# Performance work log

Measured on AMD Instinct MI355X. Metric: run time of the kernel, lower is better.

Reference implementation:

```python
import jax, jax.numpy as jnp
import numpy as np

B, C, H, W = 2, 512, 64, 64
G = 32          # GroupNorm groups
EPS = 1e-6


def setup_inputs() -> dict:
    key = jax.random.key(0)
    ks = jax.random.split(key, 10)
    s = 1.0 / np.sqrt(C)
    return {
        "x": jax.random.normal(ks[0], (B, C, H, W), dtype=jnp.float32),
        "gn_w": jnp.ones((C,), jnp.float32),
        "gn_b": jnp.zeros((C,), jnp.float32),
        "wq": jax.random.normal(ks[1], (C, C), jnp.float32) * s,
        "bq": jnp.zeros((C,), jnp.float32),
        "wk": jax.random.normal(ks[2], (C, C), jnp.float32) * s,
        "bk": jnp.zeros((C,), jnp.float32),
        "wv": jax.random.normal(ks[3], (C, C), jnp.float32) * s,
        "bv": jnp.zeros((C,), jnp.float32),
        "wo": jax.random.normal(ks[4], (C, C), jnp.float32) * s,
        "bo": jnp.zeros((C,), jnp.float32),
    }


def reference(x, gn_w, gn_b, wq, bq, wk, bk, wv, bv, wo, bo):
    b, c, h, w = x.shape
    n = h * w
    # GroupNorm(32, eps=1e-6, affine)
    xg = x.reshape(b, G, c // G, h, w)
    mu = xg.mean(axis=(2, 3, 4), keepdims=True)
    var = ((xg - mu) ** 2).mean(axis=(2, 3, 4), keepdims=True)
    hn = ((xg - mu) * jax.lax.rsqrt(var + EPS)).reshape(b, c, h, w)
    hn = hn * gn_w[None, :, None, None] + gn_b[None, :, None, None]
    # 1x1 convs == per-pixel linear over channels; tokens: b n c
    hf = hn.reshape(b, c, n)
    q = jnp.einsum('oc,bcn->bno', wq, hf) + bq  # [b, n, c]
    k = jnp.einsum('oc,bcn->bno', wk, hf) + bk
    v = jnp.einsum('oc,bcn->bno', wv, hf) + bv
    scale = jnp.asarray(c, x.dtype) ** -0.5
    att = jax.nn.softmax(jnp.einsum('bic,bjc->bij', q, k) * scale, axis=-1)
    o = jnp.einsum('bij,bjc->bic', att, v)      # [b, n, c]
    out = jnp.einsum('oc,bnc->bno', wo, o) + bo # proj_out
    return x + out.transpose(0, 2, 1).reshape(b, c, h, w)
```

## Files before the change

kernel.cpp:

```cpp
#include <hip/hip_runtime.h>
#include <hip/hip_bf16.h>


typedef float f32x4 __attribute__((ext_vector_type(4)));
typedef __bf16 bf16x8 __attribute__((ext_vector_type(8)));

typedef const __attribute__((address_space(1))) unsigned char* gas_p;
typedef __attribute__((address_space(3))) unsigned char* las_p;

__device__ __forceinline__ void gload_lds16(const void* g, void* l) {
  __builtin_amdgcn_global_load_lds((gas_p)g, (las_p)l, 16, 0, 0);
}

__global__ __launch_bounds__(256) void gn_stats_k(const float* __restrict__ x,
                                                  float* __restrict__ stats) {
  int bg = blockIdx.x;
  const float4* p = (const float4*)(x + (size_t)bg * 65536);
  float s = 0.f, s2 = 0.f;
  for (int i = threadIdx.x; i < 16384; i += 256) {
    float4 v = p[i];
    s  += v.x + v.y + v.z + v.w;
    s2 += v.x * v.x + v.y * v.y + v.z * v.z + v.w * v.w;
  }
#pragma unroll
  for (int off = 32; off > 0; off >>= 1) {
    s  += __shfl_xor(s, off);
    s2 += __shfl_xor(s2, off);
  }
  __shared__ float rs[4], rs2[4];
  int wid = threadIdx.x >> 6, lane = threadIdx.x & 63;
  if (lane == 0) { rs[wid] = s; rs2[wid] = s2; }
  __syncthreads();
  if (threadIdx.x == 0) {
    float S  = rs[0] + rs[1] + rs[2] + rs[3];
    float S2 = rs2[0] + rs2[1] + rs2[2] + rs2[3];
    float mean = S * (1.f / 65536.f);
    float var  = S2 * (1.f / 65536.f) - mean * mean;
    stats[bg * 2]     = mean;
    stats[bg * 2 + 1] = rsqrtf(var + 1e-6f);
  }
}

__global__ __launch_bounds__(256) void gn_apply_k(const float* __restrict__ x,
                                                  const float* __restrict__ stats,
                                                  const float* __restrict__ gw,
                                                  const float* __restrict__ gb,
                                                  __hip_bfloat16* __restrict__ hf) {
  int c0 = blockIdx.x * 64, n0 = blockIdx.y * 64, b = blockIdx.z;
  __shared__ float tile[64][65];
  int tx = threadIdx.x & 63, ty = threadIdx.x >> 6;
  const float* xb = x + ((size_t)(b * 512 + c0)) * 4096 + n0;
#pragma unroll
  for (int i = 0; i < 64; i += 4) {
    int cl = i + ty;
    int c  = c0 + cl;
    float mean = stats[(b * 32 + (c >> 4)) * 2];
    float rstd = stats[(b * 32 + (c >> 4)) * 2 + 1];
    float v = xb[(size_t)cl * 4096 + tx];
    tile[cl][tx] = (v - mean) * rstd * gw[c] + gb[c];
  }
  __syncthreads();
  __hip_bfloat16* o = hf + ((size_t)(b * 4096 + n0)) * 512 + c0;
#pragma unroll
  for (int i = 0; i < 64; i += 4) {
    int nl = i + ty;
    o[(size_t)nl * 512 + tx] = __float2bfloat16(tile[tx][nl]);
  }
}

__global__ __launch_bounds__(256) void cvt_k(const float* __restrict__ w,
                                             __hip_bfloat16* __restrict__ o, int n) {
  int i = blockIdx.x * 256 + threadIdx.x;
  if (i < n) o[i] = __float2bfloat16(w[i]);
}

__global__ __launch_bounds__(256) void bcat_k(const float* __restrict__ bq,
                                              const float* __restrict__ bk,
                                              float* __restrict__ bqk) {
  int i = blockIdx.x * 256 + threadIdx.x;
  if (i < 512) bqk[i] = bq[i];
  else if (i < 1024) bqk[i] = bk[i - 512];
}

__global__ __launch_bounds__(256) void sum32_k(const float* __restrict__ psums,
                                               float* __restrict__ rowsum) {
  int i = blockIdx.x * 256 + threadIdx.x;
  float s = 0.f;
#pragma unroll
  for (int j = 0; j < 32; j++) s += psums[(size_t)j * 8192 + i];
  rowsum[i] = s;
}

__global__ __launch_bounds__(256, 4) void qkv_k(
    const __hip_bfloat16* __restrict__ hf, const __hip_bfloat16* __restrict__ wqk,
    const __hip_bfloat16* __restrict__ wv, const float* __restrict__ bqk,
    const float* __restrict__ bv, __hip_bfloat16* __restrict__ qk,
    __hip_bfloat16* __restrict__ vT) {
  bool isV = blockIdx.x >= 8;
  int m0 = isV ? (blockIdx.x - 8) * 128 : blockIdx.y * 128;
  int n0 = isV ? blockIdx.y * 128 : blockIdx.x * 128;
  const __hip_bfloat16* A  = isV ? wv : hf;
  const __hip_bfloat16* Bm = isV ? hf : wqk;

  __shared__ __align__(16) unsigned char smem[34816];
  __hip_bfloat16* As  = (__hip_bfloat16*)smem;
  __hip_bfloat16* Bs  = As + 8192;
  __hip_bfloat16* epi = (__hip_bfloat16*)smem;

  int tid  = threadIdx.x;
  int wvx  = tid >> 6, lane = tid & 63;
  int wr   = (wvx >> 1) * 64, wc = (wvx & 1) * 64;
  int quad = lane >> 4, l16 = lane & 15;

  int srow = wvx * 32 + (lane >> 2);
  int scol = (lane & 3) * 8;
  const __hip_bfloat16* gA0 = A  + (size_t)(m0 + srow) * 512 + scol;
  const __hip_bfloat16* gA1 = gA0 + (size_t)16 * 512;
  const __hip_bfloat16* gB0 = Bm + (size_t)(n0 + srow) * 512 + scol;
  const __hip_bfloat16* gB1 = gB0 + (size_t)16 * 512;

  auto stage = [&](int kk, int bsel) {
    int lb = bsel * 4096 + wvx * 1024;
    gload_lds16(gA0 + kk, &As[lb]);
    gload_lds16(gA1 + kk, &As[lb + 512]);
    gload_lds16(gB0 + kk, &Bs[lb]);
    gload_lds16(gB1 + kk, &Bs[lb + 512]);
  };

  f32x4 acc[4][4] = {};
  stage(0, 0);
  for (int kt = 0; kt < 16; kt++) {
    __syncthreads();
    if (kt + 1 < 16) stage((kt + 1) << 5, (kt + 1) & 1);
    const __hip_bfloat16* Ab = &As[(kt & 1) * 4096];
    const __hip_bfloat16* Bb = &Bs[(kt & 1) * 4096];
    bf16x8 af[4], bfr[4];
#pragma unroll
    for (int i = 0; i < 4; i++)
      af[i] = *(const bf16x8*)&Ab[(wr + i * 16 + l16) * 32 + quad * 8];
#pragma unroll
    for (int j = 0; j < 4; j++)
      bfr[j] = *(const bf16x8*)&Bb[(wc + j * 16 + l16) * 32 + quad * 8];
#pragma unroll
    for (int i = 0; i < 4; i++)
#pragma unroll
      for (int j = 0; j < 4; j++)
        acc[i][j] = __builtin_amdgcn_mfma_f32_16x16x32_bf16(af[i], bfr[j],
                                                            acc[i][j], 0, 0, 0);
  }

  float bj[4], bm[4][4];
  if (!isV) {
#pragma unroll
    for (int j = 0; j < 4; j++) bj[j] = bqk[n0 + wc + j * 16 + l16];
  } else {
#pragma unroll
    for (int i = 0; i < 4; i++)
#pragma unroll
      for (int r = 0; r < 4; r++)
        bm[i][r] = bv[m0 + wr + i * 16 + quad * 4 + r];
  }
  __syncthreads();
#pragma unroll
  for (int i = 0; i < 4; i++)
#pragma unroll
    for (int j = 0; j < 4; j++)
#pragma unroll
      for (int r = 0; r < 4; r++) {
        int ml = wr + i * 16 + quad * 4 + r;
        int nl = wc + j * 16 + l16;
        float v = acc[i][j][r] + (isV ? bm[i][r] : bj[j]);
        epi[ml * 136 + nl] = __float2bfloat16(v);
      }
  __syncthreads();
  int mr = tid >> 1, h = tid & 1;
  const __hip_bfloat16* rowp = &epi[mr * 136 + h * 64];
  if (!isV) {
    __hip_bfloat16* o = qk + (size_t)(m0 + mr) * 1024 + n0 + h * 64;
#pragma unroll
    for (int c = 0; c < 8; c++)
      *(uint4*)(o + c * 8) = *(const uint4*)(rowp + c * 8);
  } else {
    int b = (n0 + h * 64) >> 12, t = (n0 + h * 64) & 4095;
    __hip_bfloat16* o = vT + ((size_t)(b * 512 + m0 + mr)) * 4096 + t;
#pragma unroll
    for (int c = 0; c < 8; c++)
      *(uint4*)(o + c * 8) = *(const uint4*)(rowp + c * 8);
  }
}

template <int MODE>
__global__ __launch_bounds__(256, 4) void gemm_bt_k(
    const __hip_bfloat16* __restrict__ A, const __hip_bfloat16* __restrict__ Bm,
    void* __restrict__ Cout, const float* __restrict__ bias,
    const float* __restrict__ resid, float* __restrict__ rowsum, int Kc,
    int lda, int ldb, int ldc, float scale, long sAz, long sBz, long sCz,
    int kspl) {
  int bx, by, bz;
  if (MODE == 3) {
    int f = blockIdx.x;
    int xcd = f & 7, s = f >> 3;
    bx = s & 3;
    int g = xcd + 8 * (s >> 2);
    by = g & 31;
    bz = g >> 5;
  } else {
    bx = blockIdx.x; by = blockIdx.y; bz = blockIdx.z;
  }
  int bb = bz / kspl, ks = bz - bb * kspl;
  A  += (size_t)bb * sAz + (size_t)ks * Kc;
  Bm += (size_t)bb * sBz + (size_t)ks * Kc;
  size_t cbase = (size_t)bz * sCz;
  int m0 = by * 128, n0 = bx * 128;

  __shared__ __align__(16) unsigned char smem[34816];
  __hip_bfloat16* As  = (__hip_bfloat16*)smem;
  __hip_bfloat16* Bs  = As + 8192;
  __hip_bfloat16* epi = (__hip_bfloat16*)smem;
  float* psum2 = (float*)(smem + 32768);

  int tid  = threadIdx.x;
  int wv   = tid >> 6, lane = tid & 63;
  int wr   = (wv >> 1) * 64, wc = (wv & 1) * 64;
  int quad = lane >> 4, l16 = lane & 15;

  int srow = wv * 32 + (lane >> 2);
  int scol = (lane & 3) * 8;
  const __hip_bfloat16* gA0 = A  + (size_t)(m0 + srow) * lda + scol;
  const __hip_bfloat16* gA1 = gA0 + (size_t)16 * lda;
  const __hip_bfloat16* gB0 = Bm + (size_t)(n0 + srow) * ldb + scol;
  const __hip_bfloat16* gB1 = gB0 + (size_t)16 * ldb;

  auto stage = [&](int kk, int bsel) {
    int lb = bsel * 4096 + wv * 1024;
    gload_lds16(gA0 + kk, &As[lb]);
    gload_lds16(gA1 + kk, &As[lb + 512]);
    gload_lds16(gB0 + kk, &Bs[lb]);
    gload_lds16(gB1 + kk, &Bs[lb + 512]);
  };

  int KT = Kc >> 5;
  f32x4 acc[4][4] = {};
  stage(0, 0);
  for (int kt = 0; kt < KT; kt++) {
    __syncthreads();
    if (kt + 1 < KT) stage((kt + 1) << 5, (kt + 1) & 1);
    const __hip_bfloat16* Ab = &As[(kt & 1) * 4096];
    const __hip_bfloat16* Bb = &Bs[(kt & 1) * 4096];
    bf16x8 af[4], bfr[4];
#pragma unroll
    for (int i = 0; i < 4; i++)
      af[i] = *(const bf16x8*)&Ab[(wr + i * 16 + l16) * 32 + quad * 8];
#pragma unroll
    for (int j = 0; j < 4; j++)
      bfr[j] = *(const bf16x8*)&Bb[(wc + j * 16 + l16) * 32 + quad * 8];
#pragma unroll
    for (int i = 0; i < 4; i++)
#pragma unroll
      for (int j = 0; j < 4; j++)
        acc[i][j] = __builtin_amdgcn_mfma_f32_16x16x32_bf16(af[i], bfr[j],
                                                            acc[i][j], 0, 0, 0);
  }

  if (MODE == 2) {
    float s[4][4];
#pragma unroll
    for (int i = 0; i < 4; i++)
#pragma unroll
      for (int r = 0; r < 4; r++) s[i][r] = 0.f;
    __hip_bfloat16* o = (__hip_bfloat16*)Cout;
#pragma unroll
    for (int i = 0; i < 4; i++)
#pragma unroll
      for (int j = 0; j < 4; j++)
#pragma unroll
        for (int r = 0; r < 4; r++) {
          int m = m0 + wr + i * 16 + quad * 4 + r;
          int n = n0 + wc + j * 16 + l16;
          float v = __expf(acc[i][j][r] * scale);
          o[cbase + (size_t)m * ldc + n] = __float2bfloat16(v);
          s[i][r] += v;
        }
#pragma unroll
    for (int off = 1; off < 16; off <<= 1)
#pragma unroll
      for (int i = 0; i < 4; i++)
#pragma unroll
        for (int r = 0; r < 4; r++) s[i][r] += __shfl_xor(s[i][r], off);
    if (l16 == 0) {
#pragma unroll
      for (int i = 0; i < 4; i++)
#pragma unroll
        for (int r = 0; r < 4; r++)
          psum2[(wv & 1) * 128 + wr + i * 16 + quad * 4 + r] = s[i][r];
    }
    __syncthreads();
    if (tid < 128) {
      float v = psum2[tid] + psum2[128 + tid];
      rowsum[(size_t)bx * 8192 + bb * 4096 + m0 + tid] = v;
    }
    return;
  }

  float pre[4][4];
  if (MODE == 3) {
#pragma unroll
    for (int i = 0; i < 4; i++)
#pragma unroll
      for (int r = 0; r < 4; r++)
        pre[i][r] = 1.f / rowsum[bb * 4096 + m0 + wr + i * 16 + quad * 4 + r];
  } else {
#pragma unroll
    for (int i = 0; i < 4; i++)
#pragma unroll
      for (int r = 0; r < 4; r++)
        pre[i][r] = bias[m0 + wr + i * 16 + quad * 4 + r];
  }
  __syncthreads();
#pragma unroll
  for (int i = 0; i < 4; i++)
#pragma unroll
    for (int j = 0; j < 4; j++)
#pragma unroll
      for (int r = 0; r < 4; r++) {
        int ml = wr + i * 16 + quad * 4 + r;
        int nl = wc + j * 16 + l16;
        float v = acc[i][j][r];
        if (MODE == 3) v *= pre[i][r];
        else v += pre[i][r];
        epi[ml * 136 + nl] = __float2bfloat16(v);
      }
  __syncthreads();
  int mr = tid >> 1, h = tid & 1;
  const __hip_bfloat16* rowp = &epi[mr * 136 + h * 64];
  size_t obase = cbase + (size_t)(m0 + mr) * ldc + n0 + h * 64;
  if (MODE == 3) {
    __hip_bfloat16* o = (__hip_bfloat16*)Cout + obase;
#pragma unroll
    for (int c = 0; c < 8; c++)
      *(uint4*)(o + c * 8) = *(const uint4*)(rowp + c * 8);
  } else {
    float* o = (float*)Cout;
#pragma unroll
    for (int c = 0; c < 8; c++) {
      bf16x8 val = *(const bf16x8*)(rowp + c * 8);
      size_t idx = obase + c * 8;
      float4 r0 = *(const float4*)&resid[idx];
      float4 r1 = *(const float4*)&resid[idx + 4];
      float4 o0, o1;
      o0.x = r0.x + (float)val[0]; o0.y = r0.y + (float)val[1];
      o0.z = r0.z + (float)val[2]; o0.w = r0.w + (float)val[3];
      o1.x = r1.x + (float)val[4]; o1.y = r1.y + (float)val[5];
      o1.z = r1.z + (float)val[6]; o1.w = r1.w + (float)val[7];
      *(float4*)&o[idx] = o0;
      *(float4*)&o[idx + 4] = o1;
    }
  }
}

__global__ __launch_bounds__(256) void reduce_k(const __hip_bfloat16* __restrict__ part,
                                                __hip_bfloat16* __restrict__ obuf) {
  size_t i8 = (size_t)blockIdx.x * 256 + threadIdx.x;
  size_t perb = (size_t)4096 * 512 / 8;
  size_t b = i8 / perb, r = i8 - b * perb;
  float acc[8] = {};
#pragma unroll
  for (int ks = 0; ks < 4; ks++) {
    bf16x8 v = ((const bf16x8*)part)[(b * 4 + ks) * perb + r];
#pragma unroll
    for (int l = 0; l < 8; l++) acc[l] += (float)v[l];
  }
  bf16x8 o;
#pragma unroll
  for (int l = 0; l < 8; l++) o[l] = (__bf16)acc[l];
  ((bf16x8*)obuf)[b * perb + r] = o;
}

extern "C" void kernel_launch(void* const* d_in, const int* in_sizes, int n_in,
                              void* d_out, int out_size, void* d_ws,
                              size_t ws_size, hipStream_t stream) {
  const float* xp  = (const float*)d_in[0];
  const float* gwp = (const float*)d_in[1];
  const float* gbp = (const float*)d_in[2];
  const float* wqp = (const float*)d_in[3];
  const float* bqp = (const float*)d_in[4];
  const float* wkp = (const float*)d_in[5];
  const float* bkp = (const float*)d_in[6];
  const float* wvp = (const float*)d_in[7];
  const float* bvp = (const float*)d_in[8];
  const float* wop = (const float*)d_in[9];
  const float* bop = (const float*)d_in[10];
  float* outp = (float*)d_out;

  char* w = (char*)d_ws;
  size_t off = 0;
  auto alloc = [&](size_t bytes) {
    void* p = w + off;
    off += (bytes + 255) & ~(size_t)255;
    return p;
  };
  float* stats         = (float*)alloc(64 * 2 * sizeof(float));
  __hip_bfloat16* hf   = (__hip_bfloat16*)alloc((size_t)2 * 4096 * 512 * 2);
  __hip_bfloat16* wqkb = (__hip_bfloat16*)alloc((size_t)1024 * 512 * 2);
  __hip_bfloat16* wvb  = (__hip_bfloat16*)alloc((size_t)512 * 512 * 2);
  __hip_bfloat16* wob  = (__hip_bfloat16*)alloc((size_t)512 * 512 * 2);
  float* bqk           = (float*)alloc(1024 * sizeof(float));
  float* rowsum        = (float*)alloc(8192 * sizeof(float));
  float* psums         = (float*)alloc((size_t)32 * 8192 * sizeof(float));
  __hip_bfloat16* qk   = (__hip_bfloat16*)alloc((size_t)2 * 4096 * 1024 * 2);
  __hip_bfloat16* vT   = (__hip_bfloat16*)alloc((size_t)2 * 512 * 4096 * 2);
  __hip_bfloat16* obuf = (__hip_bfloat16*)alloc((size_t)2 * 4096 * 512 * 2);
  __hip_bfloat16* part = (__hip_bfloat16*)alloc((size_t)8 * 4096 * 512 * 2);
  __hip_bfloat16* Sbuf = (__hip_bfloat16*)alloc((size_t)2 * 4096 * 4096 * 2);

  const int NW = 262144;
  const int CVG = (NW + 255) / 256;

  gn_stats_k<<<64, 256, 0, stream>>>(xp, stats);
  gn_apply_k<<<dim3(8, 64, 2), 256, 0, stream>>>(xp, stats, gwp, gbp, hf);
  cvt_k<<<CVG, 256, 0, stream>>>(wqp, wqkb, NW);
  cvt_k<<<CVG, 256, 0, stream>>>(wkp, wqkb + NW, NW);
  cvt_k<<<CVG, 256, 0, stream>>>(wvp, wvb, NW);
  cvt_k<<<CVG, 256, 0, stream>>>(wop, wob, NW);
  bcat_k<<<4, 256, 0, stream>>>(bqp, bkp, bqk);

  qkv_k<<<dim3(12, 64, 1), 256, 0, stream>>>(hf, wqkb, wvb, bqk, bvp, qk, vT);

  gemm_bt_k<2><<<dim3(32, 32, 2), 256, 0, stream>>>(
      qk, qk + 512, Sbuf, nullptr, nullptr, psums, 512, 1024, 1024, 4096,
      0.044194173824159216f, (long)4096 * 1024, (long)4096 * 1024,
      (long)4096 * 4096, 1);

  sum32_k<<<32, 256, 0, stream>>>(psums, rowsum);

  gemm_bt_k<3><<<dim3(1024, 1, 1), 256, 0, stream>>>(
      Sbuf, vT, part, nullptr, nullptr, rowsum, 1024, 4096, 4096, 512, 1.f,
      (long)4096 * 4096, (long)512 * 4096, (long)4096 * 512, 4);

  reduce_k<<<2048, 256, 0, stream>>>(part, obuf);

  gemm_bt_k<6><<<dim3(32, 4, 2), 256, 0, stream>>>(
      wob, obuf, outp, bop, xp, nullptr, 512, 512, 512, 4096, 1.f,
      0, (long)4096 * 512, (long)512 * 4096, 1);
}
```

Baseline: 286.7 us.

## Merge prelude kernels, halve P@V split-K, fold softmax normalization into reduce

Combines the four weight-conversion launches, the bias concat and the GroupNorm stats into one prelude kernel to cut launch overhead. The P@V GEMM goes from split-K 4 to split-K 2 (512 blocks), which halves the partial buffer traffic. The 1/rowsum softmax normalization moves from the GEMM epilogue into the reduce kernel. The trade-off is fewer blocks for the GEMM (less parallelism), and rounding changes because unnormalized partials are now stored in bf16.

```diff
diff --git a/kernel.cpp b/kernel.cpp
--- a/kernel.cpp
+++ b/kernel.cpp
@@ -12,33 +12,55 @@
   __builtin_amdgcn_global_load_lds((gas_p)g, (las_p)l, 16, 0, 0);
 }
 
-__global__ __launch_bounds__(256) void gn_stats_k(const float* __restrict__ x,
-                                                  float* __restrict__ stats) {
-  int bg = blockIdx.x;
-  const float4* p = (const float4*)(x + (size_t)bg * 65536);
-  float s = 0.f, s2 = 0.f;
-  for (int i = threadIdx.x; i < 16384; i += 256) {
-    float4 v = p[i];
-    s  += v.x + v.y + v.z + v.w;
-    s2 += v.x * v.x + v.y * v.y + v.z * v.z + v.w * v.w;
-  }
-#pragma unroll
-  for (int off = 32; off > 0; off >>= 1) {
-    s  += __shfl_xor(s, off);
-    s2 += __shfl_xor(s2, off);
-  }
-  __shared__ float rs[4], rs2[4];
-  int wid = threadIdx.x >> 6, lane = threadIdx.x & 63;
-  if (lane == 0) { rs[wid] = s; rs2[wid] = s2; }
-  __syncthreads();
-  if (threadIdx.x == 0) {
-    float S  = rs[0] + rs[1] + rs[2] + rs[3];
-    float S2 = rs2[0] + rs2[1] + rs2[2] + rs2[3];
-    float mean = S * (1.f / 65536.f);
-    float var  = S2 * (1.f / 65536.f) - mean * mean;
-    stats[bg * 2]     = mean;
-    stats[bg * 2 + 1] = rsqrtf(var + 1e-6f);
-  }
+__global__ __launch_bounds__(256) void prelude_k(
+    const float* __restrict__ wq, const float* __restrict__ wk,
+    const float* __restrict__ wv, const float* __restrict__ wo,
+    __hip_bfloat16* __restrict__ wqkb, __hip_bfloat16* __restrict__ wvb,
+    __hip_bfloat16* __restrict__ wob, const float* __restrict__ bq,
+    const float* __restrict__ bk, float* __restrict__ bqk,
+    const float* __restrict__ x, float* __restrict__ stats) {
+  int bid = blockIdx.x;
+  if (bid < 4096) {
+    const float* src;
+    __hip_bfloat16* dst;
+    if (bid < 1024)      { src = wq; dst = wqkb; }
+    else if (bid < 2048) { src = wk; dst = wqkb + 262144; }
+    else if (bid < 3072) { src = wv; dst = wvb; }
+    else                 { src = wo; dst = wob; }
+    int i = (bid & 1023) * 256 + threadIdx.x;
+    dst[i] = __float2bfloat16(src[i]);
+    return;
+  }
+  if (bid < 4160) {
+    int bg = bid - 4096;
+    const float4* p = (const float4*)(x + (size_t)bg * 65536);
+    float s = 0.f, s2 = 0.f;
+    for (int i = threadIdx.x; i < 16384; i += 256) {
+      float4 v = p[i];
+      s  += v.x + v.y + v.z + v.w;
+      s2 += v.x * v.x + v.y * v.y + v.z * v.z + v.w * v.w;
+    }
+#pragma unroll
+    for (int off = 32; off > 0; off >>= 1) {
+      s  += __shfl_xor(s, off);
+      s2 += __shfl_xor(s2, off);
+    }
+    __shared__ float rs[4], rs2[4];
+    int wid = threadIdx.x >> 6, lane = threadIdx.x & 63;
+    if (lane == 0) { rs[wid] = s; rs2[wid] = s2; }
+    __syncthreads();
+    if (threadIdx.x == 0) {
+      float S  = rs[0] + rs[1] + rs[2] + rs[3];
+      float S2 = rs2[0] + rs2[1] + rs2[2] + rs2[3];
+      float mean = S * (1.f / 65536.f);
+      float var  = S2 * (1.f / 65536.f) - mean * mean;
+      stats[bg * 2]     = mean;
+      stats[bg * 2 + 1] = rsqrtf(var + 1e-6f);
+    }
+    return;
+  }
+  for (int j = threadIdx.x; j < 1024; j += 256)
+    bqk[j] = (j < 512) ? bq[j] : bk[j - 512];
 }
 
 __global__ __launch_bounds__(256) void gn_apply_k(const float* __restrict__ x,
@@ -66,20 +88,6 @@
     int nl = i + ty;
     o[(size_t)nl * 512 + tx] = __float2bfloat16(tile[tx][nl]);
   }
-}
-
-__global__ __launch_bounds__(256) void cvt_k(const float* __restrict__ w,
-                                             __hip_bfloat16* __restrict__ o, int n) {
-  int i = blockIdx.x * 256 + threadIdx.x;
-  if (i < n) o[i] = __float2bfloat16(w[i]);
-}
-
-__global__ __launch_bounds__(256) void bcat_k(const float* __restrict__ bq,
-                                              const float* __restrict__ bk,
-                                              float* __restrict__ bqk) {
-  int i = blockIdx.x * 256 + threadIdx.x;
-  if (i < 512) bqk[i] = bq[i];
-  else if (i < 1024) bqk[i] = bk[i - 512];
 }
 
 __global__ __launch_bounds__(256) void sum32_k(const float* __restrict__ psums,
@@ -303,13 +311,7 @@
   }
 
   float pre[4][4];
-  if (MODE == 3) {
-#pragma unroll
-    for (int i = 0; i < 4; i++)
-#pragma unroll
-      for (int r = 0; r < 4; r++)
-        pre[i][r] = 1.f / rowsum[bb * 4096 + m0 + wr + i * 16 + quad * 4 + r];
-  } else {
+  if (MODE == 6) {
 #pragma unroll
     for (int i = 0; i < 4; i++)
 #pragma unroll
@@ -326,8 +328,7 @@
         int ml = wr + i * 16 + quad * 4 + r;
         int nl = wc + j * 16 + l16;
         float v = acc[i][j][r];
-        if (MODE == 3) v *= pre[i][r];
-        else v += pre[i][r];
+        if (MODE == 6) v += pre[i][r];
         epi[ml * 136 + nl] = __float2bfloat16(v);
       }
   __syncthreads();
@@ -359,20 +360,22 @@
 }
 
 __global__ __launch_bounds__(256) void reduce_k(const __hip_bfloat16* __restrict__ part,
+                                                const float* __restrict__ rowsum,
                                                 __hip_bfloat16* __restrict__ obuf) {
   size_t i8 = (size_t)blockIdx.x * 256 + threadIdx.x;
   size_t perb = (size_t)4096 * 512 / 8;
   size_t b = i8 / perb, r = i8 - b * perb;
+  float inv = 1.f / rowsum[b * 4096 + (r >> 6)];
   float acc[8] = {};
 #pragma unroll
-  for (int ks = 0; ks < 4; ks++) {
-    bf16x8 v = ((const bf16x8*)part)[(b * 4 + ks) * perb + r];
+  for (int ks = 0; ks < 2; ks++) {
+    bf16x8 v = ((const bf16x8*)part)[(b * 2 + ks) * perb + r];
 #pragma unroll
     for (int l = 0; l < 8; l++) acc[l] += (float)v[l];
   }
   bf16x8 o;
 #pragma unroll
-  for (int l = 0; l < 8; l++) o[l] = (__bf16)acc[l];
+  for (int l = 0; l < 8; l++) o[l] = (__bf16)(acc[l] * inv);
   ((bf16x8*)obuf)[b * perb + r] = o;
 }
 
@@ -410,19 +413,13 @@
   __hip_bfloat16* qk   = (__hip_bfloat16*)alloc((size_t)2 * 4096 * 1024 * 2);
   __hip_bfloat16* vT   = (__hip_bfloat16*)alloc((size_t)2 * 512 * 4096 * 2);
   __hip_bfloat16* obuf = (__hip_bfloat16*)alloc((size_t)2 * 4096 * 512 * 2);
-  __hip_bfloat16* part = (__hip_bfloat16*)alloc((size_t)8 * 4096 * 512 * 2);
+  __hip_bfloat16* part = (__hip_bfloat16*)alloc((size_t)4 * 4096 * 512 * 2);
   __hip_bfloat16* Sbuf = (__hip_bfloat16*)alloc((size_t)2 * 4096 * 4096 * 2);
 
-  const int NW = 262144;
-  const int CVG = (NW + 255) / 256;
-
-  gn_stats_k<<<64, 256, 0, stream>>>(xp, stats);
+  prelude_k<<<4161, 256, 0, stream>>>(wqp, wkp, wvp, wop, wqkb, wvb, wob,
+                                      bqp, bkp, bqk, xp, stats);
+
   gn_apply_k<<<dim3(8, 64, 2), 256, 0, stream>>>(xp, stats, gwp, gbp, hf);
-  cvt_k<<<CVG, 256, 0, stream>>>(wqp, wqkb, NW);
-  cvt_k<<<CVG, 256, 0, stream>>>(wkp, wqkb + NW, NW);
-  cvt_k<<<CVG, 256, 0, stream>>>(wvp, wvb, NW);
-  cvt_k<<<CVG, 256, 0, stream>>>(wop, wob, NW);
-  bcat_k<<<4, 256, 0, stream>>>(bqp, bkp, bqk);
 
   qkv_k<<<dim3(12, 64, 1), 256, 0, stream>>>(hf, wqkb, wvb, bqk, bvp, qk, vT);
 
@@ -433,11 +430,11 @@
 
   sum32_k<<<32, 256, 0, stream>>>(psums, rowsum);
 
-  gemm_bt_k<3><<<dim3(1024, 1, 1), 256, 0, stream>>>(
-      Sbuf, vT, part, nullptr, nullptr, rowsum, 1024, 4096, 4096, 512, 1.f,
-      (long)4096 * 4096, (long)512 * 4096, (long)4096 * 512, 4);
-
-  reduce_k<<<2048, 256, 0, stream>>>(part, obuf);
+  gemm_bt_k<3><<<dim3(512, 1, 1), 256, 0, stream>>>(
+      Sbuf, vT, part, nullptr, nullptr, nullptr, 2048, 4096, 4096, 512, 1.f,
+      (long)4096 * 4096, (long)512 * 4096, (long)4096 * 512, 2);
+
+  reduce_k<<<2048, 256, 0, stream>>>(part, rowsum, obuf);
 
   gemm_bt_k<6><<<dim3(32, 4, 2), 256, 0, stream>>>(
       wob, obuf, outp, bop, xp, nullptr, 512, 512, 512, 4096, 1.f,
```

After: 270.0 us. 1.06x faster.
